# Performance work log

Measured on AMD Instinct MI355X. Metric: run time of the kernel, lower is better.

The kernel has to match this reference:

```python
import jax, jax.numpy as jnp
import numpy as np

HEADS = 16
DIM_HEAD = 64
NUM_W = 4  # num_adaptive_weights
SCALE = DIM_HEAD ** -0.5


def setup_inputs() -> dict:
    key = jax.random.key(0)
    k0, k1, k2, k3 = jax.random.split(key, 4)
    b, n, dim = 2, 2048, 1024
    dim_inner = HEADS * DIM_HEAD  # 1024
    x = jax.random.normal(k0, (b, n, dim), jnp.float32)
    # Linear weights stored as (in, out); torch Linear(in,out,bias=False) computes x @ W.T
    Wqkv = jax.random.normal(k1, (dim, dim_inner * 3 * NUM_W), jnp.float32) * (dim ** -0.5)
    Wg = jax.random.normal(k2, (dim, NUM_W), jnp.float32) * (dim ** -0.5)
    Wout = jax.random.normal(k3, (dim_inner, dim * NUM_W), jnp.float32) * (dim_inner ** -0.5)
    mask = jnp.ones((b, n), dtype=bool)
    return {"x": x, "Wqkv": Wqkv, "Wg": Wg, "Wout": Wout, "mask": mask}


def reference(x, Wqkv, Wg, Wout, mask):
    b, n, dim = x.shape
    # to_qkv: packed last dim order is (qkv, h, d, w) per Rearrange 'b n (qkv h d w) -> qkv b h n d w'
    qkv = (x @ Wqkv).reshape(b, n, 3, HEADS, DIM_HEAD, NUM_W)
    qkv = jnp.transpose(qkv, (2, 0, 3, 1, 4, 5))  # [3, b, h, n, d, w]
    # adaptive gates: softmax over the w adaptive weights
    gates = jax.nn.softmax(x @ Wg, axis=-1)  # [b, n, w]
    # gated sum over adaptive-weight axis
    qkv = jnp.einsum('qbhndw,bnw->qbhnd', qkv, gates)
    q, k, v = qkv[0] * SCALE, qkv[1], qkv[2]
    sim = jnp.einsum('bhid,bhjd->bhij', q, k)  # [b, h, n, n]
    sim = jnp.where(mask[:, None, None, :], sim, jnp.finfo(sim.dtype).min)
    attn = jax.nn.softmax(sim, axis=-1)
    out = jnp.einsum('bhij,bhjd->bhid', attn, v)  # [b, h, n, d]
    out = out.transpose(0, 2, 1, 3).reshape(b, n, HEADS * DIM_HEAD)  # 'b h n d -> b n (h d)'
    out = (out @ Wout).reshape(b, n, dim, NUM_W)  # 'b n (d w) -> b n d w'
    # gated sum over w for the output projection
    return jnp.einsum('bndw,bnw->bnd', out, gates)
```

## Files before the change

kernel.cpp:

```cpp
#include <hip/hip_runtime.h>
#include <hip/hip_bf16.h>

#define M_TOT 4096
#define DIM_  1024
#define KP    4096
#define NC1   3072
#define NC2   1024

typedef unsigned short u16;
typedef unsigned int u32;
typedef unsigned long long u64;
typedef short bf16x8 __attribute__((ext_vector_type(8)));
typedef float f32x4 __attribute__((ext_vector_type(4)));

#define QSCALE 0.18033688011112042f
#define EXPOFF 20.0f

static __device__ __forceinline__ u16 f2bf(float f) {
    union { float f; u32 u; } v; v.f = f;
    u32 u = v.u;
    u += 0x7fffu + ((u >> 16) & 1u);
    return (u16)(u >> 16);
}
static __device__ __forceinline__ float bf2f(u16 h) {
    union { u32 u; float f; } v; v.u = ((u32)h) << 16; return v.f;
}

static __device__ __forceinline__ void gld_lds16(const u16* g, u16* l) {
    __builtin_amdgcn_global_load_lds(
        (__attribute__((address_space(1))) void*)(u64)g,
        (__attribute__((address_space(3))) void*)(u32)(u64)l,
        16, 0, 0);
}

#define SWZ_SCOL(lane) ((((lane) & 7) ^ (((lane) >> 3) & 7)) * 8)

#define RAW_BARRIER()   asm volatile("s_barrier" ::: "memory")
#define WAIT_VM0()      asm volatile("s_waitcnt vmcnt(0)" ::: "memory")
#define WAIT_LGKM0()    asm volatile("s_waitcnt lgkmcnt(0)" ::: "memory")

__global__ __launch_bounds__(256) void pre_kernel(const float* __restrict__ x,
                                                  const float* __restrict__ Wg,
                                                  const float* __restrict__ Wqkv,
                                                  float* __restrict__ gates,
                                                  u16* __restrict__ outA,
                                                  u16* __restrict__ B1) {
    __shared__ u16 lds[64 * 68];
    const int t = threadIdx.x;
    if (blockIdx.x < 192) {
        const int cg0 = blockIdx.x * 16, k0 = blockIdx.y * 64;
        const float4* s4 = (const float4*)Wqkv;
        for (int i = 0; i < 4; ++i) {
            int f = i * 256 + t;
            int kl = f >> 4, f4 = f & 15;
            float4 v = s4[(size_t)(k0 + kl) * 3072 + cg0 + f4];
            ushort4 o; o.x = f2bf(v.x); o.y = f2bf(v.y); o.z = f2bf(v.z); o.w = f2bf(v.w);
            *(ushort4*)&lds[kl * 68 + f4 * 4] = o;
        }
        __syncthreads();
        ushort4* d4 = (ushort4*)B1;
        for (int i = 0; i < 4; ++i) {
            int j = i * 256 + t;
            int cgl = j >> 6, kl = j & 63;
            d4[(size_t)(cg0 + cgl) * 1024 + k0 + kl] = *(ushort4*)&lds[kl * 68 + cgl * 4];
        }
    } else {
        const int wid = t >> 6, lane = t & 63;
        const int gb = (blockIdx.x - 192) * 16 + blockIdx.y;
        const int m = gb * 4 + wid;
        const float* xr = x + (size_t)m * DIM_;
        float a0 = 0.f, a1 = 0.f, a2 = 0.f, a3 = 0.f;
        for (int i = 0; i < DIM_ / 64; ++i) {
            int k = i * 64 + lane;
            float xv = xr[k];
            float4 wg = ((const float4*)Wg)[k];
            a0 += xv * wg.x; a1 += xv * wg.y; a2 += xv * wg.z; a3 += xv * wg.w;
        }
        for (int s = 1; s < 64; s <<= 1) {
            a0 += __shfl_xor(a0, s); a1 += __shfl_xor(a1, s);
            a2 += __shfl_xor(a2, s); a3 += __shfl_xor(a3, s);
        }
        float mx = fmaxf(fmaxf(a0, a1), fmaxf(a2, a3));
        float e0 = __expf(a0 - mx), e1 = __expf(a1 - mx), e2 = __expf(a2 - mx), e3 = __expf(a3 - mx);
        float inv = 1.0f / (e0 + e1 + e2 + e3);
        float g0 = e0 * inv, g1 = e1 * inv, g2 = e2 * inv, g3 = e3 * inv;
        if (lane == 0) ((float4*)gates)[m] = make_float4(g0, g1, g2, g3);
        ushort4* out4 = (ushort4*)outA;
        for (int i = 0; i < DIM_ / 64; ++i) {
            int k = i * 64 + lane;
            float val = xr[k];
            ushort4 o;
            o.x = f2bf(val * g0); o.y = f2bf(val * g1); o.z = f2bf(val * g2); o.w = f2bf(val * g3);
            out4[(size_t)m * 1024 + k] = o;
        }
    }
}

__global__ __launch_bounds__(256) void bprep_kernel(const float* __restrict__ src,
                                                    u16* __restrict__ dst,
                                                    int R, int Cg) {
    __shared__ u16 lds[64 * 68];
    const int t = threadIdx.x;
    const int cg0 = blockIdx.x * 16, k0 = blockIdx.y * 64;
    const float4* s4 = (const float4*)src;
    for (int i = 0; i < 4; ++i) {
        int f = i * 256 + t;
        int kl = f >> 4, f4 = f & 15;
        float4 v = s4[(size_t)(k0 + kl) * Cg + cg0 + f4];
        ushort4 o; o.x = f2bf(v.x); o.y = f2bf(v.y); o.z = f2bf(v.z); o.w = f2bf(v.w);
        *(ushort4*)&lds[kl * 68 + f4 * 4] = o;
    }
    __syncthreads();
    ushort4* d4 = (ushort4*)dst;
    for (int i = 0; i < 4; ++i) {
        int j = i * 256 + t;
        int cgl = j >> 6, kl = j & 63;
        d4[(size_t)(cg0 + cgl) * R + k0 + kl] = *(ushort4*)&lds[kl * 68 + cgl * 4];
    }
}

__global__ __launch_bounds__(256) void gemm1_kernel(const u16* __restrict__ A,
                                                    const u16* __restrict__ Bm,
                                                    u16* __restrict__ qbuf,
                                                    u16* __restrict__ kbuf,
                                                    u16* __restrict__ vbuf) {
    __shared__ u16 lA[128 * 64];
    __shared__ u16 lB[128 * 64];
    const int t = threadIdx.x;
    const int lane = t & 63, wid = t >> 6;
    const int wm = wid >> 1, wn = wid & 1;
    const int l15 = lane & 15, quad = lane >> 4;
    const int sx = l15 & 7;
    const int n0 = blockIdx.x * 128, m0 = blockIdx.y * 128;
    const int srow = lane >> 3, scol = SWZ_SCOL(lane);
    const u16* gA = A + (size_t)(m0 + wid * 32 + srow) * KP + scol;
    const u16* gB = Bm + (size_t)(n0 + wid * 32 + srow) * KP + scol;
    u16* lAw = &lA[wid * 2048];
    u16* lBw = &lB[wid * 2048];
    f32x4 acc[4][4] = {};
    for (int k0 = 0; k0 < KP; k0 += 64) {
        for (int i = 0; i < 4; ++i)
            gld_lds16(gA + (size_t)i * 8 * KP + k0, lAw + i * 512);
        for (int i = 0; i < 4; ++i)
            gld_lds16(gB + (size_t)i * 8 * KP + k0, lBw + i * 512);
        __syncthreads();
        for (int ks = 0; ks < 2; ++ks) {
            const int co = ((ks * 4 + quad) ^ sx) * 8;
            bf16x8 af[4], bfr[4];
            for (int mt = 0; mt < 4; ++mt)
                af[mt] = *(const bf16x8*)&lA[(wm * 64 + mt * 16 + l15) * 64 + co];
            for (int nt = 0; nt < 4; ++nt)
                bfr[nt] = *(const bf16x8*)&lB[(wn * 64 + nt * 16 + l15) * 64 + co];
            for (int mt = 0; mt < 4; ++mt)
                for (int nt = 0; nt < 4; ++nt)
                    acc[mt][nt] = __builtin_amdgcn_mfma_f32_16x16x32_bf16(af[mt], bfr[nt], acc[mt][nt], 0, 0, 0);
        }
        __syncthreads();
    }
    const int qkv = n0 >> 10;
    const int base_hd = n0 & 1023;
    for (int mt = 0; mt < 4; ++mt) {
        int mrow = m0 + wm * 64 + mt * 16 + quad * 4;
        int b = mrow >> 11, n = mrow & 2047;
        int bh0 = b * 16;
        for (int nt = 0; nt < 4; ++nt) {
            int hd = base_hd + wn * 64 + nt * 16 + l15;
            int h = hd >> 6, d = hd & 63;
            int bh = bh0 + h;
            if (qkv == 0) {
                for (int r = 0; r < 4; ++r)
                    qbuf[((size_t)bh * 2048 + n + r) * 64 + d] = f2bf(acc[mt][nt][r] * QSCALE);
            } else if (qkv == 1) {
                for (int r = 0; r < 4; ++r)
                    kbuf[((size_t)bh * 2048 + n + r) * 64 + d] = f2bf(acc[mt][nt][r]);
            } else {
                ushort4 o;
                o.x = f2bf(acc[mt][nt][0]); o.y = f2bf(acc[mt][nt][1]);
                o.z = f2bf(acc[mt][nt][2]); o.w = f2bf(acc[mt][nt][3]);
                *(ushort4*)&vbuf[((size_t)bh * 64 + d) * 2048 + n] = o;
            }
        }
    }
}

__global__ __launch_bounds__(256) void gemm2_kernel(const u16* __restrict__ A,
                                                    const u16* __restrict__ Bm,
                                                    float* __restrict__ outf) {
    __shared__ u16 lA[2][128 * 64];
    __shared__ u16 lB[2][64 * 64];
    const int t = threadIdx.x;
    const int lane = t & 63, wid = t >> 6;
    const int wm = wid >> 1, wn = wid & 1;
    const int l15 = lane & 15, quad = lane >> 4;
    const int sx = l15 & 7;
    const int bid0 = blockIdx.y * 16 + blockIdx.x;
    const int nbid = (bid0 & 7) * 64 + (bid0 >> 3);
    const int n0 = (nbid & 15) * 64, m0 = (nbid >> 4) * 128;
    const int srow = lane >> 3, scol = SWZ_SCOL(lane);
    const u16* gA = A + (size_t)(m0 + wid * 32 + srow) * KP + scol;
    const u16* gB = Bm + (size_t)(n0 + wid * 16 + srow) * KP + scol;
    for (int i = 0; i < 4; ++i)
        gld_lds16(gA + (size_t)i * 8 * KP, &lA[0][(wid * 32 + i * 8) * 64]);
    for (int i = 0; i < 2; ++i)
        gld_lds16(gB + (size_t)i * 8 * KP, &lB[0][(wid * 16 + i * 8) * 64]);
    f32x4 acc[4][2] = {};
    for (int it = 0; it < 64; ++it) {
        const int cur = it & 1;
        WAIT_VM0();
        RAW_BARRIER();
        if (it + 1 < 64) {
            const int k0 = (it + 1) * 64, nb = cur ^ 1;
            for (int i = 0; i < 4; ++i)
                gld_lds16(gA + (size_t)i * 8 * KP + k0, &lA[nb][(wid * 32 + i * 8) * 64]);
            for (int i = 0; i < 2; ++i)
                gld_lds16(gB + (size_t)i * 8 * KP + k0, &lB[nb][(wid * 16 + i * 8) * 64]);
        }
        for (int ks = 0; ks < 2; ++ks) {
            const int co = ((ks * 4 + quad) ^ sx) * 8;
            bf16x8 af[4], bfr[2];
            for (int mt = 0; mt < 4; ++mt)
                af[mt] = *(const bf16x8*)&lA[cur][(wm * 64 + mt * 16 + l15) * 64 + co];
            for (int nt = 0; nt < 2; ++nt)
                bfr[nt] = *(const bf16x8*)&lB[cur][(wn * 32 + nt * 16 + l15) * 64 + co];
            for (int mt = 0; mt < 4; ++mt)
                for (int nt = 0; nt < 2; ++nt)
                    acc[mt][nt] = __builtin_amdgcn_mfma_f32_16x16x32_bf16(af[mt], bfr[nt], acc[mt][nt], 0, 0, 0);
        }
    }
    for (int mt = 0; mt < 4; ++mt) {
        int mrow = m0 + wm * 64 + mt * 16 + quad * 4;
        for (int nt = 0; nt < 2; ++nt) {
            int col = n0 + wn * 32 + nt * 16 + l15;
            for (int r = 0; r < 4; ++r)
                outf[(size_t)(mrow + r) * NC2 + col] = acc[mt][nt][r];
        }
    }
}

__global__ __launch_bounds__(256) void attn_kernel(const u16* __restrict__ qbuf,
                                                   const u16* __restrict__ kbuf,
                                                   const u16* __restrict__ vbuf,
                                                   const float* __restrict__ gates,
                                                   u16* __restrict__ outA) {
    __shared__ u16 lK[2][64 * 64];
    __shared__ u16 lV[2][64 * 64];
    __shared__ u16 lP[4][2 * 16 * 72];
    const int t = threadIdx.x, lane = t & 63, wq = t >> 6;
    const int l15 = lane & 15, quad = lane >> 4;
    const int sx7 = l15 & 7;
    const int bid0 = blockIdx.y * 16 + blockIdx.x;
    const int nbid = (bid0 & 7) * 64 + (bid0 >> 3);
    const int bh = nbid >> 4, q0 = (nbid & 15) * 128;
    const u16* Q = qbuf + (size_t)bh * 2048 * 64;
    const u16* K = kbuf + (size_t)bh * 2048 * 64;
    const u16* V = vbuf + (size_t)bh * 64 * 2048;
    bf16x8 qf[2][2];
    for (int mt = 0; mt < 2; ++mt)
        for (int ks = 0; ks < 2; ++ks)
            qf[mt][ks] = *(const bf16x8*)&Q[(size_t)(q0 + wq * 32 + mt * 16 + l15) * 64 + ks * 32 + quad * 8];
    f32x4 Oa[2][4] = {};
    float lacc[2] = {0.f, 0.f};
    const int krow = lane >> 3, kcol = SWZ_SCOL(lane);
    const u16* gK = K + (size_t)(wq * 16 + krow) * 64 + kcol;
    const u16* gV = V + (size_t)(wq * 16 + krow) * 2048 + kcol;
    u16* lPw = lP[wq];
    gld_lds16(gK, &lK[0][(wq * 16) * 64]);
    gld_lds16(gK + (size_t)8 * 64, &lK[0][(wq * 16 + 8) * 64]);
    gld_lds16(gV, &lV[0][(wq * 16) * 64]);
    gld_lds16(gV + (size_t)8 * 2048, &lV[0][(wq * 16 + 8) * 64]);
    for (int kt = 0; kt < 32; ++kt) {
        const int cur = kt & 1;
        WAIT_VM0();
        RAW_BARRIER();
        if (kt + 1 < 32) {
            const int nxt = (kt + 1) * 64, nb = cur ^ 1;
            gld_lds16(gK + (size_t)nxt * 64, &lK[nb][(wq * 16) * 64]);
            gld_lds16(gK + (size_t)(nxt + 8) * 64, &lK[nb][(wq * 16 + 8) * 64]);
            gld_lds16(gV + nxt, &lV[nb][(wq * 16) * 64]);
            gld_lds16(gV + nxt + (size_t)8 * 2048, &lV[nb][(wq * 16 + 8) * 64]);
        }
        f32x4 S[2][4] = {};
        for (int ks = 0; ks < 2; ++ks) {
            const int co = ((ks * 4 + quad) ^ sx7) * 8;
            for (int nt = 0; nt < 4; ++nt) {
                bf16x8 kf = *(const bf16x8*)&lK[cur][(nt * 16 + l15) * 64 + co];
                S[0][nt] = __builtin_amdgcn_mfma_f32_16x16x32_bf16(kf, qf[0][ks], S[0][nt], 0, 0, 0);
                S[1][nt] = __builtin_amdgcn_mfma_f32_16x16x32_bf16(kf, qf[1][ks], S[1][nt], 0, 0, 0);
            }
        }
        for (int mt = 0; mt < 2; ++mt) {
            u16* lPm = lPw + mt * (16 * 72);
            for (int nt = 0; nt < 4; ++nt) {
                float p0 = __builtin_amdgcn_exp2f(S[mt][nt][0] - EXPOFF);
                float p1 = __builtin_amdgcn_exp2f(S[mt][nt][1] - EXPOFF);
                float p2 = __builtin_amdgcn_exp2f(S[mt][nt][2] - EXPOFF);
                float p3 = __builtin_amdgcn_exp2f(S[mt][nt][3] - EXPOFF);
                lacc[mt] += (p0 + p1) + (p2 + p3);
                uint2 pk;
                pk.x = (u32)f2bf(p0) | ((u32)f2bf(p1) << 16);
                pk.y = (u32)f2bf(p2) | ((u32)f2bf(p3) << 16);
                *(uint2*)&lPm[l15 * 72 + nt * 16 + quad * 4] = pk;
            }
        }
        WAIT_LGKM0();
        for (int ks = 0; ks < 2; ++ks) {
            const int co = ((ks * 4 + quad) ^ sx7) * 8;
            bf16x8 p0 = *(const bf16x8*)&lPw[0 * (16 * 72) + l15 * 72 + ks * 32 + quad * 8];
            bf16x8 p1 = *(const bf16x8*)&lPw[1 * (16 * 72) + l15 * 72 + ks * 32 + quad * 8];
            for (int dt = 0; dt < 4; ++dt) {
                bf16x8 vf = *(const bf16x8*)&lV[cur][(dt * 16 + l15) * 64 + co];
                Oa[0][dt] = __builtin_amdgcn_mfma_f32_16x16x32_bf16(p0, vf, Oa[0][dt], 0, 0, 0);
                Oa[1][dt] = __builtin_amdgcn_mfma_f32_16x16x32_bf16(p1, vf, Oa[1][dt], 0, 0, 0);
            }
        }
    }
    for (int mt = 0; mt < 2; ++mt) {
        lacc[mt] += __shfl_xor(lacc[mt], 16);
        lacc[mt] += __shfl_xor(lacc[mt], 32);
    }
    const int b = bh >> 4, h = bh & 15;
    ushort4* out4 = (ushort4*)outA;
    const float4* gates4 = (const float4*)gates;
    for (int mt = 0; mt < 2; ++mt) {
        for (int r = 0; r < 4; ++r) {
            int n = q0 + wq * 32 + mt * 16 + quad * 4 + r;
            int m = b * 2048 + n;
            float invl = 1.0f / __shfl(lacc[mt], quad * 4 + r);
            float4 g = gates4[m];
            for (int dt = 0; dt < 4; ++dt) {
                float val = Oa[mt][dt][r] * invl;
                ushort4 o;
                o.x = f2bf(val * g.x); o.y = f2bf(val * g.y);
                o.z = f2bf(val * g.z); o.w = f2bf(val * g.w);
                out4[(size_t)m * 1024 + h * 64 + dt * 16 + l15] = o;
            }
        }
    }
}

extern "C" void kernel_launch(void* const* d_in, const int* in_sizes, int n_in,
                              void* d_out, int out_size, void* d_ws, size_t ws_size,
                              hipStream_t stream) {
    const float* x    = (const float*)d_in[0];
    const float* Wqkv = (const float*)d_in[1];
    const float* Wg   = (const float*)d_in[2];
    const float* Wout = (const float*)d_in[3];

    char* ws = (char*)d_ws;
    size_t off = 0;
    float* gates = (float*)(ws + off); off += (size_t)1 << 16;
    u16* Aexp = (u16*)(ws + off);      off += (size_t)M_TOT * KP * 2;
    char* regB = ws + off;             off += (size_t)NC1 * KP * 2;
    u16* B1 = (u16*)regB;
    u16* B2 = (u16*)(regB + (size_t)M_TOT * NC2 * 2);
    u16* qbuf = (u16*)(ws + off); off += (size_t)32 * 2048 * 64 * 2;
    u16* kbuf = (u16*)(ws + off); off += (size_t)32 * 2048 * 64 * 2;
    u16* vbuf = (u16*)(ws + off); off += (size_t)32 * 2048 * 64 * 2;

    hipLaunchKernelGGL(pre_kernel, dim3(256, 16), dim3(256), 0, stream,
                       x, Wg, Wqkv, gates, Aexp, B1);
    hipLaunchKernelGGL(gemm1_kernel, dim3(24, 32), dim3(256), 0, stream,
                       Aexp, B1, qbuf, kbuf, vbuf);
    hipLaunchKernelGGL(bprep_kernel, dim3(64, 16), dim3(256), 0, stream,
                       Wout, B2, 1024, 1024);
    hipLaunchKernelGGL(attn_kernel, dim3(16, 32), dim3(256), 0, stream,
                       qbuf, kbuf, vbuf, gates, Aexp);
    hipLaunchKernelGGL(gemm2_kernel, dim3(16, 32), dim3(256), 0, stream,
                       Aexp, B2, (float*)d_out);
}
```

Baseline: 359.7 us.

## Apply output gates after gemm2 instead of expanding attention output by gates

Previously the attention output was expanded four times (once per adaptive weight, pre-multiplied by the gates) into a K=4096 activation, and gemm2 ran against a pre-summed weight matrix. Now attention writes a plain 1024-wide output, gemm2 multiplies it by the full transposed Wout (N=4096, K=1024), and the gated sum over w is done in the epilogue via lane shuffles. The FLOP count is unchanged, but the activation traffic and attention-epilogue writes shrink. The cost is a wider output grid and a shuffle reduction in the epilogue.

```diff
diff --git a/kernel.cpp b/kernel.cpp
--- a/kernel.cpp
+++ b/kernel.cpp
@@ -21,9 +21,6 @@
     u32 u = v.u;
     u += 0x7fffu + ((u >> 16) & 1u);
     return (u16)(u >> 16);
-}
-static __device__ __forceinline__ float bf2f(u16 h) {
-    union { u32 u; float f; } v; v.u = ((u32)h) << 16; return v.f;
 }
 
 static __device__ __forceinline__ void gld_lds16(const u16* g, u16* l) {
@@ -96,26 +93,27 @@
     }
 }
 
-__global__ __launch_bounds__(256) void bprep_kernel(const float* __restrict__ src,
-                                                    u16* __restrict__ dst,
-                                                    int R, int Cg) {
+__global__ __launch_bounds__(256) void wtrans_kernel(const float* __restrict__ src,
+                                                     u16* __restrict__ dst) {
     __shared__ u16 lds[64 * 68];
     const int t = threadIdx.x;
-    const int cg0 = blockIdx.x * 16, k0 = blockIdx.y * 64;
+    const int c0 = blockIdx.x * 64, r0 = blockIdx.y * 64;
     const float4* s4 = (const float4*)src;
     for (int i = 0; i < 4; ++i) {
         int f = i * 256 + t;
-        int kl = f >> 4, f4 = f & 15;
-        float4 v = s4[(size_t)(k0 + kl) * Cg + cg0 + f4];
-        ushort4 o; o.x = f2bf(v.x); o.y = f2bf(v.y); o.z = f2bf(v.z); o.w = f2bf(v.w);
-        *(ushort4*)&lds[kl * 68 + f4 * 4] = o;
+        int rl = f >> 4, f4 = f & 15;
+        float4 v = s4[(size_t)(r0 + rl) * 1024 + (c0 >> 2) + f4];
+        lds[(f4 * 4 + 0) * 68 + rl] = f2bf(v.x);
+        lds[(f4 * 4 + 1) * 68 + rl] = f2bf(v.y);
+        lds[(f4 * 4 + 2) * 68 + rl] = f2bf(v.z);
+        lds[(f4 * 4 + 3) * 68 + rl] = f2bf(v.w);
     }
     __syncthreads();
     ushort4* d4 = (ushort4*)dst;
     for (int i = 0; i < 4; ++i) {
         int j = i * 256 + t;
-        int cgl = j >> 6, kl = j & 63;
-        d4[(size_t)(cg0 + cgl) * R + k0 + kl] = *(ushort4*)&lds[kl * 68 + cgl * 4];
+        int cl = j >> 4, r4 = j & 15;
+        d4[(size_t)(c0 + cl) * 256 + (r0 >> 2) + r4] = *(ushort4*)&lds[cl * 68 + r4 * 4];
     }
 }
 
@@ -183,8 +181,9 @@
     }
 }
 
-__global__ __launch_bounds__(256) void gemm2_kernel(const u16* __restrict__ A,
-                                                    const u16* __restrict__ Bm,
+__global__ __launch_bounds__(256) void gemm2_kernel(const u16* __restrict__ O,
+                                                    const u16* __restrict__ Bn,
+                                                    const float* __restrict__ gates,
                                                     float* __restrict__ outf) {
     __shared__ u16 lA[2][128 * 64];
     __shared__ u16 lB[2][64 * 64];
@@ -193,27 +192,27 @@
     const int wm = wid >> 1, wn = wid & 1;
     const int l15 = lane & 15, quad = lane >> 4;
     const int sx = l15 & 7;
-    const int bid0 = blockIdx.y * 16 + blockIdx.x;
-    const int nbid = (bid0 & 7) * 64 + (bid0 >> 3);
-    const int n0 = (nbid & 15) * 64, m0 = (nbid >> 4) * 128;
+    const int bid0 = blockIdx.y * 64 + blockIdx.x;
+    const int nbid = (bid0 & 7) * 256 + (bid0 >> 3);
+    const int n0 = (nbid & 63) * 64, m0 = (nbid >> 6) * 128;
     const int srow = lane >> 3, scol = SWZ_SCOL(lane);
-    const u16* gA = A + (size_t)(m0 + wid * 32 + srow) * KP + scol;
-    const u16* gB = Bm + (size_t)(n0 + wid * 16 + srow) * KP + scol;
+    const u16* gA = O + (size_t)(m0 + wid * 32 + srow) * 1024 + scol;
+    const u16* gB = Bn + (size_t)(n0 + wid * 16 + srow) * 1024 + scol;
     for (int i = 0; i < 4; ++i)
-        gld_lds16(gA + (size_t)i * 8 * KP, &lA[0][(wid * 32 + i * 8) * 64]);
+        gld_lds16(gA + (size_t)i * 8 * 1024, &lA[0][(wid * 32 + i * 8) * 64]);
     for (int i = 0; i < 2; ++i)
-        gld_lds16(gB + (size_t)i * 8 * KP, &lB[0][(wid * 16 + i * 8) * 64]);
+        gld_lds16(gB + (size_t)i * 8 * 1024, &lB[0][(wid * 16 + i * 8) * 64]);
     f32x4 acc[4][2] = {};
-    for (int it = 0; it < 64; ++it) {
+    for (int it = 0; it < 16; ++it) {
         const int cur = it & 1;
         WAIT_VM0();
         RAW_BARRIER();
-        if (it + 1 < 64) {
+        if (it + 1 < 16) {
             const int k0 = (it + 1) * 64, nb = cur ^ 1;
             for (int i = 0; i < 4; ++i)
-                gld_lds16(gA + (size_t)i * 8 * KP + k0, &lA[nb][(wid * 32 + i * 8) * 64]);
+                gld_lds16(gA + (size_t)i * 8 * 1024 + k0, &lA[nb][(wid * 32 + i * 8) * 64]);
             for (int i = 0; i < 2; ++i)
-                gld_lds16(gB + (size_t)i * 8 * KP + k0, &lB[nb][(wid * 16 + i * 8) * 64]);
+                gld_lds16(gB + (size_t)i * 8 * 1024 + k0, &lB[nb][(wid * 16 + i * 8) * 64]);
         }
         for (int ks = 0; ks < 2; ++ks) {
             const int co = ((ks * 4 + quad) ^ sx) * 8;
@@ -229,10 +228,17 @@
     }
     for (int mt = 0; mt < 4; ++mt) {
         int mrow = m0 + wm * 64 + mt * 16 + quad * 4;
-        for (int nt = 0; nt < 2; ++nt) {
-            int col = n0 + wn * 32 + nt * 16 + l15;
-            for (int r = 0; r < 4; ++r)
-                outf[(size_t)(mrow + r) * NC2 + col] = acc[mt][nt][r];
+        for (int r = 0; r < 4; ++r) {
+            float gv = gates[(size_t)(mrow + r) * 4 + (lane & 3)];
+            for (int nt = 0; nt < 2; ++nt) {
+                float v = acc[mt][nt][r] * gv;
+                v += __shfl_xor(v, 1);
+                v += __shfl_xor(v, 2);
+                if ((lane & 3) == 0) {
+                    int col = n0 + wn * 32 + nt * 16 + l15;
+                    outf[(size_t)(mrow + r) * NC2 + (col >> 2)] = v;
+                }
+            }
         }
     }
 }
@@ -240,8 +246,7 @@
 __global__ __launch_bounds__(256) void attn_kernel(const u16* __restrict__ qbuf,
                                                    const u16* __restrict__ kbuf,
                                                    const u16* __restrict__ vbuf,
-                                                   const float* __restrict__ gates,
-                                                   u16* __restrict__ outA) {
+                                                   u16* __restrict__ obuf) {
     __shared__ u16 lK[2][64 * 64];
     __shared__ u16 lV[2][64 * 64];
     __shared__ u16 lP[4][2 * 16 * 72];
@@ -319,21 +324,13 @@
         lacc[mt] += __shfl_xor(lacc[mt], 32);
     }
     const int b = bh >> 4, h = bh & 15;
-    ushort4* out4 = (ushort4*)outA;
-    const float4* gates4 = (const float4*)gates;
     for (int mt = 0; mt < 2; ++mt) {
         for (int r = 0; r < 4; ++r) {
             int n = q0 + wq * 32 + mt * 16 + quad * 4 + r;
             int m = b * 2048 + n;
             float invl = 1.0f / __shfl(lacc[mt], quad * 4 + r);
-            float4 g = gates4[m];
-            for (int dt = 0; dt < 4; ++dt) {
-                float val = Oa[mt][dt][r] * invl;
-                ushort4 o;
-                o.x = f2bf(val * g.x); o.y = f2bf(val * g.y);
-                o.z = f2bf(val * g.z); o.w = f2bf(val * g.w);
-                out4[(size_t)m * 1024 + h * 64 + dt * 16 + l15] = o;
-            }
+            for (int dt = 0; dt < 4; ++dt)
+                obuf[(size_t)m * 1024 + h * 64 + dt * 16 + l15] = f2bf(Oa[mt][dt][r] * invl);
         }
     }
 }
@@ -352,19 +349,20 @@
     u16* Aexp = (u16*)(ws + off);      off += (size_t)M_TOT * KP * 2;
     char* regB = ws + off;             off += (size_t)NC1 * KP * 2;
     u16* B1 = (u16*)regB;
-    u16* B2 = (u16*)(regB + (size_t)M_TOT * NC2 * 2);
+    u16* Bn = (u16*)(regB + ((size_t)8 << 20));
     u16* qbuf = (u16*)(ws + off); off += (size_t)32 * 2048 * 64 * 2;
     u16* kbuf = (u16*)(ws + off); off += (size_t)32 * 2048 * 64 * 2;
     u16* vbuf = (u16*)(ws + off); off += (size_t)32 * 2048 * 64 * 2;
+    u16* obuf = (u16*)(ws + off); off += (size_t)M_TOT * 1024 * 2;
 
     hipLaunchKernelGGL(pre_kernel, dim3(256, 16), dim3(256), 0, stream,
                        x, Wg, Wqkv, gates, Aexp, B1);
     hipLaunchKernelGGL(gemm1_kernel, dim3(24, 32), dim3(256), 0, stream,
                        Aexp, B1, qbuf, kbuf, vbuf);
-    hipLaunchKernelGGL(bprep_kernel, dim3(64, 16), dim3(256), 0, stream,
-                       Wout, B2, 1024, 1024);
+    hipLaunchKernelGGL(wtrans_kernel, dim3(64, 16), dim3(256), 0, stream,
+                       Wout, Bn);
     hipLaunchKernelGGL(attn_kernel, dim3(16, 32), dim3(256), 0, stream,
-                       qbuf, kbuf, vbuf, gates, Aexp);
-    hipLaunchKernelGGL(gemm2_kernel, dim3(16, 32), dim3(256), 0, stream,
-                       Aexp, B2, (float*)d_out);
-}
+                       qbuf, kbuf, vbuf, obuf);
+    hipLaunchKernelGGL(gemm2_kernel, dim3(64, 32), dim3(256), 0, stream,
+                       obuf, Bn, gates, (float*)d_out);
+}
```

Result: slower. 374.4 us (+4.1%).

## Double-buffer gemm1 LDS tiles with K=32 stages to overlap loads and MFMA

Applied to the files above, without the earlier changes.

Restructures the QKV projection GEMM main loop to use two LDS buffers with 32-wide K tiles. The next stage is prefetched while MFMAs run on the current one, replacing two barriers per iteration with one wait plus a barrier. This hides global-to-LDS load latency behind compute. The trade-off is a new swizzle pattern, twice as many loop iterations, and a stall on vmcnt(0) every iteration. The B2 offset expression is rewritten to an equivalent constant.

```diff
diff --git a/kernel.cpp b/kernel.cpp
--- a/kernel.cpp
+++ b/kernel.cpp
@@ -21,9 +21,6 @@
     u32 u = v.u;
     u += 0x7fffu + ((u >> 16) & 1u);
     return (u16)(u >> 16);
-}
-static __device__ __forceinline__ float bf2f(u16 h) {
-    union { u32 u; float f; } v; v.u = ((u32)h) << 16; return v.f;
 }
 
 static __device__ __forceinline__ void gld_lds16(const u16* g, u16* l) {
@@ -124,39 +121,50 @@
                                                     u16* __restrict__ qbuf,
                                                     u16* __restrict__ kbuf,
                                                     u16* __restrict__ vbuf) {
-    __shared__ u16 lA[128 * 64];
-    __shared__ u16 lB[128 * 64];
+    __shared__ u16 lA[2][128 * 32];
+    __shared__ u16 lB[2][128 * 32];
     const int t = threadIdx.x;
     const int lane = t & 63, wid = t >> 6;
     const int wm = wid >> 1, wn = wid & 1;
     const int l15 = lane & 15, quad = lane >> 4;
-    const int sx = l15 & 7;
+    const int sw = (l15 >> 1) & 3;
     const int n0 = blockIdx.x * 128, m0 = blockIdx.y * 128;
-    const int srow = lane >> 3, scol = SWZ_SCOL(lane);
+    const int srow = lane >> 2;
+    const int scol = (((lane & 3) ^ ((lane >> 3) & 3)) * 8);
     const u16* gA = A + (size_t)(m0 + wid * 32 + srow) * KP + scol;
     const u16* gB = Bm + (size_t)(n0 + wid * 32 + srow) * KP + scol;
-    u16* lAw = &lA[wid * 2048];
-    u16* lBw = &lB[wid * 2048];
+
+#define G1_STAGE(tt, ss) do {                                              \
+        const size_t _k = (size_t)(tt) * 32;                               \
+        gld_lds16(gA + _k,                   &lA[ss][(wid * 32) * 32]);      \
+        gld_lds16(gA + _k + (size_t)16 * KP, &lA[ss][(wid * 32 + 16) * 32]); \
+        gld_lds16(gB + _k,                   &lB[ss][(wid * 32) * 32]);      \
+        gld_lds16(gB + _k + (size_t)16 * KP, &lB[ss][(wid * 32 + 16) * 32]); \
+    } while (0)
+
+    G1_STAGE(0, 0);
     f32x4 acc[4][4] = {};
-    for (int k0 = 0; k0 < KP; k0 += 64) {
-        for (int i = 0; i < 4; ++i)
-            gld_lds16(gA + (size_t)i * 8 * KP + k0, lAw + i * 512);
-        for (int i = 0; i < 4; ++i)
-            gld_lds16(gB + (size_t)i * 8 * KP + k0, lBw + i * 512);
-        __syncthreads();
-        for (int ks = 0; ks < 2; ++ks) {
-            const int co = ((ks * 4 + quad) ^ sx) * 8;
-            bf16x8 af[4], bfr[4];
-            for (int mt = 0; mt < 4; ++mt)
-                af[mt] = *(const bf16x8*)&lA[(wm * 64 + mt * 16 + l15) * 64 + co];
+    const int co = (quad ^ sw) * 8;
+    for (int it = 0; it < 128; ++it) {
+        const int cur = it & 1;
+        WAIT_VM0();
+        RAW_BARRIER();
+        if (it + 1 < 128) G1_STAGE(it + 1, cur ^ 1);
+        bf16x8 af[4], bfr[4];
+#pragma unroll
+        for (int mt = 0; mt < 4; ++mt)
+            af[mt] = *(const bf16x8*)&lA[cur][(wm * 64 + mt * 16 + l15) * 32 + co];
+#pragma unroll
+        for (int nt = 0; nt < 4; ++nt)
+            bfr[nt] = *(const bf16x8*)&lB[cur][(wn * 64 + nt * 16 + l15) * 32 + co];
+#pragma unroll
+        for (int mt = 0; mt < 4; ++mt)
+#pragma unroll
             for (int nt = 0; nt < 4; ++nt)
-                bfr[nt] = *(const bf16x8*)&lB[(wn * 64 + nt * 16 + l15) * 64 + co];
-            for (int mt = 0; mt < 4; ++mt)
-                for (int nt = 0; nt < 4; ++nt)
-                    acc[mt][nt] = __builtin_amdgcn_mfma_f32_16x16x32_bf16(af[mt], bfr[nt], acc[mt][nt], 0, 0, 0);
-        }
-        __syncthreads();
-    }
+                acc[mt][nt] = __builtin_amdgcn_mfma_f32_16x16x32_bf16(af[mt], bfr[nt], acc[mt][nt], 0, 0, 0);
+    }
+#undef G1_STAGE
+
     const int qkv = n0 >> 10;
     const int base_hd = n0 & 1023;
     for (int mt = 0; mt < 4; ++mt) {
@@ -352,7 +360,7 @@
     u16* Aexp = (u16*)(ws + off);      off += (size_t)M_TOT * KP * 2;
     char* regB = ws + off;             off += (size_t)NC1 * KP * 2;
     u16* B1 = (u16*)regB;
-    u16* B2 = (u16*)(regB + (size_t)M_TOT * NC2 * 2);
+    u16* B2 = (u16*)(regB + ((size_t)8 << 20));
     u16* qbuf = (u16*)(ws + off); off += (size_t)32 * 2048 * 64 * 2;
     u16* kbuf = (u16*)(ws + off); off += (size_t)32 * 2048 * 64 * 2;
     u16* vbuf = (u16*)(ws + off); off += (size_t)32 * 2048 * 64 * 2;
```

Result: no change. 361.4 us (median of 3 runs) (+0.5%).
